# Optimization experiments

Hardware: AMD Instinct MI355X
Metric: run time of the kernel (lower is better)

The kernel has to match this reference:

```python
import jax, jax.numpy as jnp
import numpy as np

# pywt db4 decomposition low-pass filter
_DEC_LO = jnp.array([-0.010597401785069032, 0.0328830116668852, 0.030841381835560764,
                     -0.18703481171909309, -0.027983769416859854, 0.6308807679298589,
                     0.7148465705529157, 0.2303778133088965], dtype=jnp.float32)
_L = 8
_SIGN = jnp.where(jnp.arange(_L) % 2 == 0, -1.0, 1.0).astype(jnp.float32)
_DEC_HI = _SIGN * _DEC_LO[::-1]            # QMF: dec_hi[k] = (-1)^(k+1) dec_lo[L-1-k]
_REC_LO = _DEC_LO[::-1]
_REC_HI = _DEC_HI[::-1]
_LEVELS = 4


def _conv_valid(x, f):
    # x: [N, n]; true convolution (filter flipped), valid part
    k = f[::-1][None, None, :]
    return jax.lax.conv_general_dilated(x[:, None, :], k, (1,), 'VALID',
                                        dimension_numbers=('NCH', 'OIH', 'NCH'))[:, 0, :]


def _dwt(x):
    # one symmetric-mode DWT level; x: [N, n] -> (cA, cD) each [N, (n+L-1)//2]
    xp = jnp.pad(x, ((0, 0), (_L - 1, _L - 1)), mode='symmetric')
    return _conv_valid(xp, _DEC_LO)[:, 1::2], _conv_valid(xp, _DEC_HI)[:, 1::2]


def _idwt(a, d):
    # inverse DWT level; a,d: [N, m] -> [N, 2m-L+2]
    m = a.shape[-1]
    up_a = jnp.zeros((a.shape[0], 2 * m - 1), a.dtype).at[:, ::2].set(a)
    up_d = jnp.zeros((d.shape[0], 2 * m - 1), d.dtype).at[:, ::2].set(d)
    y = (_conv_valid(jnp.pad(up_a, ((0, 0), (_L - 1, _L - 1))), _REC_LO)
         + _conv_valid(jnp.pad(up_d, ((0, 0), (_L - 1, _L - 1))), _REC_HI))
    return y[:, _L - 2: y.shape[-1] - (_L - 2)]


def _wavelet_compress(x, level):
    # batched equivalent of the per-(b,c) pywt wavedec/threshold/waverec loop
    B, C, T = x.shape
    a = x.reshape(B * C, T)
    details = []
    for _ in range(_LEVELS):
        a, d = _dwt(a)
        details.append(d)
    thr = level * jnp.std(a, axis=-1, keepdims=True)  # np.std (ddof=0) of approx coeffs per row
    hard = lambda c: jnp.where(jnp.abs(c) < thr, jnp.zeros((), c.dtype), c)
    a = hard(a)
    for d in reversed(details):
        d = hard(d)
        if a.shape[-1] > d.shape[-1]:
            a = a[:, :d.shape[-1]]  # pywt waverec length alignment
        a = _idwt(a, d)
    if a.shape[-1] >= T:
        a = a[:, :T]
    else:
        a = jnp.pad(a, ((0, 0), (0, T - a.shape[-1])))
    return a.reshape(B, C, T)


def _spectral_distortion(x, key, freq_mask_prob=0.3, time_mask_prob=0.3):
    T = x.shape[-1]
    k1, k2, k3, k4 = jax.random.split(key, 4)
    X = jnp.fft.fft(x, axis=-1)
    mag, ph = jnp.abs(X), jnp.angle(X)
    idx = jnp.arange(T)
    fw = int(0.1 * T)
    f0 = jax.random.randint(k2, (), 0, T - fw)
    apply_f = jax.random.uniform(k1, ()) < freq_mask_prob
    fmask = apply_f & (idx >= f0) & (idx < f0 + fw)
    mag = mag * jnp.where(fmask, 0.1, 1.0).astype(mag.dtype)
    xd = jnp.fft.ifft(mag * jnp.exp(1j * ph), axis=-1).real.astype(x.dtype)
    tw = int(0.05 * T)
    t0 = jax.random.randint(k4, (), 0, T - tw)
    apply_t = jax.random.uniform(k3, ()) < time_mask_prob
    tmask = apply_t & (idx >= t0) & (idx < t0 + tw)
    return xd * jnp.where(tmask, 0.1, 1.0).astype(x.dtype)


def _add_noise(x, key, noise_std=0.02):
    # torch.std is unbiased -> ddof=1
    noise = jax.random.normal(key, x.shape, x.dtype) * noise_std * jnp.std(x, axis=-1, keepdims=True, ddof=1)
    return x + noise


def setup_inputs() -> dict:
    key = jax.random.key(0)
    x = jax.random.normal(key, (64, 64, 4096), dtype=jnp.float32)
    return {"x": x}


def reference(x):
    compression_level = 0.5  # fixed draw from compression_levels for determinism
    kd, kn, kcd, kcn = jax.random.split(jax.random.key(42), 4)
    compressed = _wavelet_compress(x, compression_level)
    distorted = _spectral_distortion(x, kd)
    noisy = _add_noise(x, kn)
    comb = _wavelet_compress(x, compression_level * 0.5)
    comb = _spectral_distortion(comb, kcd)
    comb = _add_noise(comb, kcn)
    # views: original, compressed, distorted, noisy, combined
    return (x, compressed, distorted, noisy, comb)
```

## Files before the change

kernel.cpp:

```cpp
#include <hip/hip_runtime.h>
#include <stdint.h>

#define T_LEN 4096
#define N_ROWS 4096
#define N_ELEM (4096u * 4096u)
#define PD(i) ((i) + ((i) >> 5))

__constant__ float c_DEC_LO[8] = {
  -0.010597401785069032f, 0.0328830116668852f, 0.030841381835560764f,
  -0.18703481171909309f, -0.027983769416859854f, 0.6308807679298589f,
   0.7148465705529157f, 0.2303778133088965f };
__constant__ float c_DEC_HI[8] = {
  -0.2303778133088965f, 0.7148465705529157f, -0.6308807679298589f,
  -0.027983769416859854f, 0.18703481171909309f, 0.030841381835560764f,
  -0.0328830116668852f, -0.010597401785069032f };

#define RL0 0.2303778133088965f
#define RL1 0.7148465705529157f
#define RL2 0.6308807679298589f
#define RL3 (-0.027983769416859854f)
#define RL4 (-0.18703481171909309f)
#define RL5 0.030841381835560764f
#define RL6 0.0328830116668852f
#define RL7 (-0.010597401785069032f)
#define RH0 (-0.010597401785069032f)
#define RH1 (-0.0328830116668852f)
#define RH2 0.030841381835560764f
#define RH3 0.18703481171909309f
#define RH4 (-0.027983769416859854f)
#define RH5 (-0.6308807679298589f)
#define RH6 0.7148465705529157f
#define RH7 (-0.2303778133088965f)

__host__ __device__ __forceinline__ uint32_t rotl32(uint32_t v, int r) {
  return (v << r) | (v >> (32 - r));
}

__host__ __device__ __forceinline__ void tf2x32(uint32_t k0, uint32_t k1,
                                                uint32_t c0, uint32_t c1,
                                                uint32_t& o0, uint32_t& o1) {
  uint32_t ks2 = k0 ^ k1 ^ 0x1BD11BDAu;
  uint32_t x0 = c0 + k0;
  uint32_t x1 = c1 + k1;
#define TFR(r) { x0 += x1; x1 = rotl32(x1, r); x1 ^= x0; }
  TFR(13) TFR(15) TFR(26) TFR(6)
  x0 += k1;  x1 += ks2 + 1u;
  TFR(17) TFR(29) TFR(16) TFR(24)
  x0 += ks2; x1 += k0 + 2u;
  TFR(13) TFR(15) TFR(26) TFR(6)
  x0 += k0;  x1 += k1 + 3u;
  TFR(17) TFR(29) TFR(16) TFR(24)
  x0 += k1;  x1 += ks2 + 4u;
  TFR(13) TFR(15) TFR(26) TFR(6)
  x0 += ks2; x1 += k0 + 5u;
#undef TFR
  o0 = x0; o1 = x1;
}

__host__ __device__ __forceinline__ uint32_t jbits_scalar(uint32_t kx, uint32_t ky) {
  uint32_t a, b; tf2x32(kx, ky, 0u, 0u, a, b);
  return a ^ b;
}

__device__ __forceinline__ uint32_t jbits_elem(uint32_t kx, uint32_t ky, uint32_t i) {
  uint32_t a, b; tf2x32(kx, ky, 0u, i, a, b); return a ^ b;
}

__host__ __device__ __forceinline__ float junif_scalar(uint32_t kx, uint32_t ky) {
  union { uint32_t u; float f; } cv;
  cv.u = (jbits_scalar(kx, ky) >> 9) | 0x3f800000u;
  return cv.f - 1.0f;
}

__host__ __device__ __forceinline__ void jsplit2(uint32_t kx, uint32_t ky, uint32_t* o) {
  tf2x32(kx, ky, 0u, 0u, o[0], o[1]);
  tf2x32(kx, ky, 0u, 1u, o[2], o[3]);
}

__host__ __device__ __forceinline__ void jsplit4(uint32_t kx, uint32_t ky, uint32_t* o) {
  tf2x32(kx, ky, 0u, 0u, o[0], o[1]);
  tf2x32(kx, ky, 0u, 1u, o[2], o[3]);
  tf2x32(kx, ky, 0u, 2u, o[4], o[5]);
  tf2x32(kx, ky, 0u, 3u, o[6], o[7]);
}

__host__ __device__ __forceinline__ int jrandint(uint32_t kx, uint32_t ky, uint32_t span) {
  uint32_t c[4];
  jsplit2(kx, ky, c);
  uint32_t hi = jbits_scalar(c[0], c[1]);
  uint32_t lo = jbits_scalar(c[2], c[3]);
  uint32_t mult = 65536u % span;
  mult = (mult * mult) % span;
  uint32_t off = ((hi % span) * mult + (lo % span)) % span;
  return (int)off;
}

__host__ __device__ void distort_params(uint32_t kx, uint32_t ky,
                                        int* f0, int* af, int* t0, int* at) {
  uint32_t q[8];
  jsplit4(kx, ky, q);
  *af = junif_scalar(q[0], q[1]) < 0.3f;
  *f0 = jrandint(q[2], q[3], 3687u);
  *at = junif_scalar(q[4], q[5]) < 0.3f;
  *t0 = jrandint(q[6], q[7], 3892u);
}

__device__ __forceinline__ float erfinv32(float x) {
  float w = -log1pf(-x * x);
  float p;
  if (w < 5.0f) {
    w = w - 2.5f;
    p = 2.81022636e-08f;
    p = fmaf(p, w, 3.43273939e-07f);
    p = fmaf(p, w, -3.5233877e-06f);
    p = fmaf(p, w, -4.39150654e-06f);
    p = fmaf(p, w, 0.00021858087f);
    p = fmaf(p, w, -0.00125372503f);
    p = fmaf(p, w, -0.00417768164f);
    p = fmaf(p, w, 0.246640727f);
    p = fmaf(p, w, 1.50140941f);
  } else {
    w = sqrtf(w) - 3.0f;
    p = -0.000200214257f;
    p = fmaf(p, w, 0.000100950558f);
    p = fmaf(p, w, 0.00134934322f);
    p = fmaf(p, w, -0.00367342844f);
    p = fmaf(p, w, 0.00573950773f);
    p = fmaf(p, w, -0.0076224613f);
    p = fmaf(p, w, 0.00943887047f);
    p = fmaf(p, w, 1.00167406f);
    p = fmaf(p, w, 2.83297682f);
  }
  return p * x;
}

__device__ __forceinline__ float jax_normal_from_bits(uint32_t bits) {
  union { uint32_t u; float f; } cv;
  cv.u = (bits >> 9) | 0x3f800000u;
  float f = cv.f - 1.0f;
  const float lo = -0.99999994f;
  float u = __fadd_rn(__fmul_rn(f, 2.0f), lo);
  u = fmaxf(lo, u);
  return 1.41421356f * erfinv32(u);
}

__device__ __forceinline__ float tree8(const float* p) {
  return __fadd_rn(
      __fadd_rn(__fadd_rn(p[0], p[1]), __fadd_rn(p[2], p[3])),
      __fadd_rn(__fadd_rn(p[4], p[5]), __fadd_rn(p[6], p[7])));
}

__device__ void dwt_step(const float* a, int n, float* oa, float* od, int nOut, int tid) {
  int iHi = (n - 2) >> 1;
  for (int i = tid; i < nOut; i += 256) {
    int base = 2 * i - 6;
    float pa[8], pd[8];
    if (i >= 3 && i <= iHi) {
      #pragma unroll
      for (int j = 0; j < 8; ++j) {
        float xv = a[base + j];
        pa[j] = __fmul_rn(c_DEC_LO[7 - j], xv);
        pd[j] = __fmul_rn(c_DEC_HI[7 - j], xv);
      }
    } else {
      #pragma unroll
      for (int j = 0; j < 8; ++j) {
        int q = base + j;
        q = (q < 0) ? (-q - 1) : ((q >= n) ? (2 * n - 1 - q) : q);
        float xv = a[q];
        pa[j] = __fmul_rn(c_DEC_LO[7 - j], xv);
        pd[j] = __fmul_rn(c_DEC_HI[7 - j], xv);
      }
    }
    oa[i] = tree8(pa);
    od[i] = tree8(pd);
  }
}

__device__ void idwt_step(const float* __restrict__ a, const float* __restrict__ d,
                          int m, float* __restrict__ out, int nOut, float thr,
                          bool trA, int tid) {
  for (int t = tid; t < nOut; t += 256) {
    int odd = t & 1;
    int h0 = (t - odd) >> 1;
    float a0 = a[h0], a1 = a[h0 + 1], a2 = a[h0 + 2], a3 = a[h0 + 3];
    if (trA) {
      a0 = (fabsf(a0) < thr) ? 0.f : a0;
      a1 = (fabsf(a1) < thr) ? 0.f : a1;
      a2 = (fabsf(a2) < thr) ? 0.f : a2;
      a3 = (fabsf(a3) < thr) ? 0.f : a3;
    }
    float d0 = d[h0], d1 = d[h0 + 1], d2 = d[h0 + 2], d3 = d[h0 + 3];
    d0 = (fabsf(d0) < thr) ? 0.f : d0;
    d1 = (fabsf(d1) < thr) ? 0.f : d1;
    d2 = (fabsf(d2) < thr) ? 0.f : d2;
    d3 = (fabsf(d3) < thr) ? 0.f : d3;
    float cl0 = odd ? RL7 : RL6, cl1 = odd ? RL5 : RL4;
    float cl2 = odd ? RL3 : RL2, cl3 = odd ? RL1 : RL0;
    float ch0 = odd ? RH7 : RH6, ch1 = odd ? RH5 : RH4;
    float ch2 = odd ? RH3 : RH2, ch3 = odd ? RH1 : RH0;
    float sa = __fadd_rn(__fadd_rn(__fmul_rn(cl0, a0), __fmul_rn(cl1, a1)),
                         __fadd_rn(__fmul_rn(cl2, a2), __fmul_rn(cl3, a3)));
    float sd = __fadd_rn(__fadd_rn(__fmul_rn(ch0, d0), __fmul_rn(ch1, d1)),
                         __fadd_rn(__fmul_rn(ch2, d2), __fmul_rn(ch3, d3)));
    out[t] = __fadd_rn(sa, sd);
  }
}

__device__ void np_pw262_partials(const float* src, float* pbuf, int tid) {
  if (tid < 24) {
    int blk = tid >> 3, k = tid & 7;
    const float* base = src + (blk == 0 ? 0 : (blk == 1 ? 128 : 192));
    int iters = (blk == 0 ? 16 : 8);
    float r = base[k];
    for (int it = 1; it < iters; ++it) r = __fadd_rn(r, base[8 * it + k]);
    pbuf[tid] = r;
  }
}

__device__ float np_pw262_combine(const float* src, const float* pbuf) {
  float b0 = tree8(pbuf + 0);
  float b1 = tree8(pbuf + 8);
  float b2 = tree8(pbuf + 16);
  for (int i = 256; i < 262; ++i) b2 = __fadd_rn(b2, src[i]);
  return __fadd_rn(b0, __fadd_rn(b1, b2));
}

__global__ __launch_bounds__(256)
void wavelet_kernel(const float* __restrict__ x, float* __restrict__ out0,
                    float* __restrict__ out1, float* __restrict__ out4,
                    int fuse, int at_c, int t0_c, uint32_t kcx, uint32_t kcy) {
  extern __shared__ float smem[];
  float* A  = smem;
  float* B  = smem + 4096;
  float* D1 = smem + 6147;
  float* D2 = smem + 8198;
  float* D3 = smem + 9227;
  float* D4 = smem + 9745;
  float* SC = smem + 10007;
  float* Bp = B + 512;
  const int row = blockIdx.x, tid = threadIdx.x;
  const float4* s4 = reinterpret_cast<const float4*>(x + (size_t)row * T_LEN);
  float4* o04 = reinterpret_cast<float4*>(out0 + (size_t)row * T_LEN);
  #pragma unroll
  for (int k = 0; k < 4; ++k) {
    float4 v = s4[tid + (k << 8)];
    *reinterpret_cast<float4*>(&A[4 * (tid + (k << 8))]) = v;
    o04[tid + (k << 8)] = v;
  }
  __syncthreads();
  dwt_step(A, 4096, B, D1, 2051, tid); __syncthreads();
  dwt_step(B, 2051, A, D2, 1029, tid); __syncthreads();
  dwt_step(A, 1029, B, D3, 518, tid);  __syncthreads();
  dwt_step(B, 518, A, D4, 262, tid);   __syncthreads();

  np_pw262_partials(A, Bp, tid);
  __syncthreads();
  if (tid == 0) SC[0] = np_pw262_combine(A, Bp) / 262.0f;
  __syncthreads();
  float mu = SC[0];
  for (int i = tid; i < 262; i += 256) {
    float dv = __fsub_rn(A[i], mu);
    B[i] = __fmul_rn(dv, dv);
  }
  __syncthreads();
  np_pw262_partials(B, Bp, tid);
  __syncthreads();
  if (tid == 0) SC[1] = __fsqrt_rn(np_pw262_combine(B, Bp) / 262.0f);
  __syncthreads();
  float sigma = SC[1];

  float ra0 = A[tid];
  float ra1 = (tid < 6) ? A[256 + tid] : 0.f;

  #pragma unroll
  for (int v = 0; v < 2; ++v) {
    if (v == 1) {
      __syncthreads();
      A[tid] = ra0;
      if (tid < 6) A[256 + tid] = ra1;
      __syncthreads();
    }
    float thr = __fmul_rn((v == 0 ? 0.5f : 0.25f), sigma);
    idwt_step(A, D4, 262, B, 518, thr, true, tid);    __syncthreads();
    idwt_step(B, D3, 518, A, 1029, thr, false, tid);  __syncthreads();
    idwt_step(A, D2, 1029, B, 2051, thr, false, tid); __syncthreads();
    idwt_step(B, D1, 2051, A, 4096, thr, false, tid); __syncthreads();
    if (v == 0) {
      float4* dst4 = reinterpret_cast<float4*>(out1 + (size_t)row * T_LEN);
      #pragma unroll
      for (int k = 0; k < 4; ++k)
        dst4[tid + (k << 8)] = *reinterpret_cast<const float4*>(&A[4 * (tid + (k << 8))]);
    }
  }

  float4* dst4 = reinterpret_cast<float4*>(out4 + (size_t)row * T_LEN);
  if (!fuse) {
    #pragma unroll
    for (int k = 0; k < 4; ++k)
      dst4[tid + (k << 8)] = *reinterpret_cast<const float4*>(&A[4 * (tid + (k << 8))]);
    return;
  }

  float w[16];
  #pragma unroll
  for (int k = 0; k < 4; ++k) {
    float4 vv = *reinterpret_cast<const float4*>(&A[4 * (tid + (k << 8))]);
    w[4 * k + 0] = vv.x; w[4 * k + 1] = vv.y; w[4 * k + 2] = vv.z; w[4 * k + 3] = vv.w;
  }
  if (at_c) {
    #pragma unroll
    for (int i = 0; i < 16; ++i) {
      int col = 4 * (tid + ((i >> 2) << 8)) + (i & 3);
      if (col >= t0_c && col < t0_c + 204) w[i] *= 0.1f;
    }
  }
  __syncthreads();
  float* red = B;
  float acc = 0.f;
  #pragma unroll
  for (int i = 0; i < 16; ++i) acc += w[i];
  red[tid] = acc; __syncthreads();
  for (int o = 128; o > 0; o >>= 1) { if (tid < o) red[tid] += red[tid + o]; __syncthreads(); }
  float nmu = red[0] * (1.0f / 4096.0f);
  __syncthreads();
  acc = 0.f;
  #pragma unroll
  for (int i = 0; i < 16; ++i) { float dv = w[i] - nmu; acc += dv * dv; }
  red[tid] = acc; __syncthreads();
  for (int o = 128; o > 0; o >>= 1) { if (tid < o) red[tid] += red[tid + o]; __syncthreads(); }
  float nsig = sqrtf(red[0] / 4095.0f);

  #pragma unroll
  for (int k = 0; k < 4; ++k) {
    float o[4];
    #pragma unroll
    for (int c = 0; c < 4; ++c) {
      uint32_t col = (uint32_t)(4 * (tid + (k << 8)) + c);
      uint32_t idx = ((uint32_t)row << 12) + col;
      float z = jax_normal_from_bits(jbits_elem(kcx, kcy, idx));
      o[c] = w[4 * k + c] + __fmul_rn(__fmul_rn(z, 0.02f), nsig);
    }
    dst4[tid + (k << 8)] = make_float4(o[0], o[1], o[2], o[3]);
  }
}

__constant__ int c_STW_OFF[6] = {0, 1024, 1280, 1344, 1360, 1364};

__global__ __launch_bounds__(256)
void distort_noise_kernel(const float* __restrict__ src, float* __restrict__ dst_d,
                          float* __restrict__ dst_n,
                          int af, int f0, int at, int t0, int nod, int wd,
                          uint32_t kx, uint32_t ky) {
  extern __shared__ float smem[];
  float* RE = smem;
  float* IM = smem + 4224;
  float2* STW = (float2*)(smem + 8448);
  const int row = blockIdx.x, tid = threadIdx.x;

  const float4* s4 = reinterpret_cast<const float4*>(src + (size_t)row * T_LEN);
  float4 v4[4];
  #pragma unroll
  for (int k = 0; k < 4; ++k) v4[k] = s4[tid + (k << 8)];

  float w[16];
  if (af) {
    for (int t = tid; t < 1365; t += 256) {
      int s, j;
      if (t < 1024) { s = 0; j = t; }
      else if (t < 1280) { s = 1; j = t - 1024; }
      else if (t < 1344) { s = 2; j = t - 1280; }
      else if (t < 1360) { s = 3; j = t - 1344; }
      else if (t < 1364) { s = 4; j = t - 1360; }
      else { s = 5; j = 0; }
      int e = j << (2 * s);
      float ang = (float)e * (-1.5339807878856412e-3f);
      float sn, cs;
      __sincosf(ang, &sn, &cs);
      STW[t] = make_float2(cs, sn);
    }
    #pragma unroll
    for (int k = 0; k < 4; ++k) {
      int p = 4 * (tid + (k << 8));
      RE[PD(p + 0)] = v4[k].x; IM[PD(p + 0)] = 0.f;
      RE[PD(p + 1)] = v4[k].y; IM[PD(p + 1)] = 0.f;
      RE[PD(p + 2)] = v4[k].z; IM[PD(p + 2)] = 0.f;
      RE[PD(p + 3)] = v4[k].w; IM[PD(p + 3)] = 0.f;
    }
    __syncthreads();
    for (int s = 0; s < 6; ++s) {
      int Lsh = 12 - 2 * s, Qsh = Lsh - 2, Qm = (1 << Qsh) - 1, off = c_STW_OFF[s];
      for (int b = tid; b < 1024; b += 256) {
        int j = b & Qm, g = b >> Qsh;
        int i0 = (g << Lsh) + j;
        int i1 = i0 + (1 << Qsh), i2 = i1 + (1 << Qsh), i3 = i2 + (1 << Qsh);
        float x0r = RE[PD(i0)], x0i = IM[PD(i0)];
        float x1r = RE[PD(i1)], x1i = IM[PD(i1)];
        float x2r = RE[PD(i2)], x2i = IM[PD(i2)];
        float x3r = RE[PD(i3)], x3i = IM[PD(i3)];
        float t0r = x0r + x2r, t0i = x0i + x2i;
        float t1r = x0r - x2r, t1i = x0i - x2i;
        float t2r = x1r + x3r, t2i = x1i + x3i;
        float t3r = x1r - x3r, t3i = x1i - x3i;
        float2 w1 = STW[off + j];
        float c1 = w1.x, s1 = w1.y;
        float c2 = c1 * c1 - s1 * s1, s2 = 2.f * c1 * s1;
        float c3 = c1 * c2 - s1 * s2, s3 = c1 * s2 + s1 * c2;
        RE[PD(i0)] = t0r + t2r; IM[PD(i0)] = t0i + t2i;
        float u1r = t1r + t3i, u1i = t1i - t3r;
        RE[PD(i1)] = u1r * c1 - u1i * s1; IM[PD(i1)] = u1r * s1 + u1i * c1;
        float u2r = t0r - t2r, u2i = t0i - t2i;
        RE[PD(i2)] = u2r * c2 - u2i * s2; IM[PD(i2)] = u2r * s2 + u2i * c2;
        float u3r = t1r - t3i, u3i = t1i + t3r;
        RE[PD(i3)] = u3r * c3 - u3i * s3; IM[PD(i3)] = u3r * s3 + u3i * c3;
      }
      __syncthreads();
    }
    for (int p = tid; p < 4096; p += 256) {
      uint32_t rb = __brev((uint32_t)p) >> 20;
      int kk = (int)(((rb & 0x555u) << 1) | ((rb >> 1) & 0x555u));
      if (kk >= f0 && kk < f0 + 409) { RE[PD(p)] *= 0.1f; IM[PD(p)] *= 0.1f; }
    }
    __syncthreads();
    for (int s = 5; s >= 0; --s) {
      int Lsh = 12 - 2 * s, Qsh = Lsh - 2, Qm = (1 << Qsh) - 1, off = c_STW_OFF[s];
      for (int b = tid; b < 1024; b += 256) {
        int j = b & Qm, g = b >> Qsh;
        int i0 = (g << Lsh) + j;
        int i1 = i0 + (1 << Qsh), i2 = i1 + (1 << Qsh), i3 = i2 + (1 << Qsh);
        float y0r = RE[PD(i0)], y0i = IM[PD(i0)];
        float y1r = RE[PD(i1)], y1i = IM[PD(i1)];
        float y2r = RE[PD(i2)], y2i = IM[PD(i2)];
        float y3r = RE[PD(i3)], y3i = IM[PD(i3)];
        float2 w1 = STW[off + j];
        float c1 = w1.x, s1 = -w1.y;
        float c2 = c1 * c1 - s1 * s1, s2 = 2.f * c1 * s1;
        float c3 = c1 * c2 - s1 * s2, s3 = c1 * s2 + s1 * c2;
        float z1r = y1r * c1 - y1i * s1, z1i = y1r * s1 + y1i * c1;
        float z2r = y2r * c2 - y2i * s2, z2i = y2r * s2 + y2i * c2;
        float z3r = y3r * c3 - y3i * s3, z3i = y3r * s3 + y3i * c3;
        float u0r = y0r + z2r, u0i = y0i + z2i;
        float u2r = y0r - z2r, u2i = y0i - z2i;
        float u1r = z1r + z3r, u1i = z1i + z3i;
        float u3r = z3i - z1i, u3i = z1r - z3r;
        RE[PD(i0)] = u0r + u1r; IM[PD(i0)] = u0i + u1i;
        RE[PD(i1)] = u2r + u3r; IM[PD(i1)] = u2i + u3i;
        RE[PD(i2)] = u0r - u1r; IM[PD(i2)] = u0i - u1i;
        RE[PD(i3)] = u2r - u3r; IM[PD(i3)] = u2i - u3i;
      }
      __syncthreads();
    }
    #pragma unroll
    for (int k = 0; k < 4; ++k) {
      int p = 4 * (tid + (k << 8));
      w[4 * k + 0] = RE[PD(p + 0)] * (1.0f / 4096.0f);
      w[4 * k + 1] = RE[PD(p + 1)] * (1.0f / 4096.0f);
      w[4 * k + 2] = RE[PD(p + 2)] * (1.0f / 4096.0f);
      w[4 * k + 3] = RE[PD(p + 3)] * (1.0f / 4096.0f);
    }
    __syncthreads();
  } else {
    #pragma unroll
    for (int k = 0; k < 4; ++k) {
      w[4 * k + 0] = v4[k].x; w[4 * k + 1] = v4[k].y;
      w[4 * k + 2] = v4[k].z; w[4 * k + 3] = v4[k].w;
    }
  }
  if (at) {
    #pragma unroll
    for (int i = 0; i < 16; ++i) {
      int col = 4 * (tid + ((i >> 2) << 8)) + (i & 3);
      if (col >= t0 && col < t0 + 204) w[i] *= 0.1f;
    }
  }
  if (wd) {
    float4* d4 = reinterpret_cast<float4*>(dst_d + (size_t)row * T_LEN);
    #pragma unroll
    for (int k = 0; k < 4; ++k)
      d4[tid + (k << 8)] = make_float4(w[4 * k], w[4 * k + 1], w[4 * k + 2], w[4 * k + 3]);
  }

  float nv[16];
  #pragma unroll
  for (int i = 0; i < 16; ++i) {
    float q;
    if (nod) q = w[i];
    else {
      float4 vv = v4[i >> 2];
      q = (i & 3) == 0 ? vv.x : (i & 3) == 1 ? vv.y : (i & 3) == 2 ? vv.z : vv.w;
    }
    nv[i] = q;
  }
  float* red = smem;
  float acc = 0.f;
  #pragma unroll
  for (int i = 0; i < 16; ++i) acc += nv[i];
  red[tid] = acc; __syncthreads();
  for (int o = 128; o > 0; o >>= 1) { if (tid < o) red[tid] += red[tid + o]; __syncthreads(); }
  float mu = red[0] * (1.0f / 4096.0f);
  __syncthreads();
  acc = 0.f;
  #pragma unroll
  for (int i = 0; i < 16; ++i) { float dv = nv[i] - mu; acc += dv * dv; }
  red[tid] = acc; __syncthreads();
  for (int o = 128; o > 0; o >>= 1) { if (tid < o) red[tid] += red[tid + o]; __syncthreads(); }
  float sigma = sqrtf(red[0] / 4095.0f);

  float4* n4 = reinterpret_cast<float4*>(dst_n + (size_t)row * T_LEN);
  #pragma unroll
  for (int k = 0; k < 4; ++k) {
    float o[4];
    #pragma unroll
    for (int c = 0; c < 4; ++c) {
      uint32_t col = (uint32_t)(4 * (tid + (k << 8)) + c);
      uint32_t idx = ((uint32_t)row << 12) + col;
      float z = jax_normal_from_bits(jbits_elem(kx, ky, idx));
      o[c] = nv[4 * k + c] + __fmul_rn(__fmul_rn(z, 0.02f), sigma);
    }
    n4[tid + (k << 8)] = make_float4(o[0], o[1], o[2], o[3]);
  }
}

extern "C" void kernel_launch(void* const* d_in, const int* in_sizes, int n_in,
                              void* d_out, int out_size, void* d_ws, size_t ws_size,
                              hipStream_t stream) {
  const float* x = (const float*)d_in[0];
  float* out = (float*)d_out;
  float* o0 = out;
  float* o1 = out + (size_t)N_ELEM;
  float* o2 = out + 2 * (size_t)N_ELEM;
  float* o3 = out + 3 * (size_t)N_ELEM;
  float* o4 = out + 4 * (size_t)N_ELEM;

  uint32_t r[8];
  jsplit4(0u, 42u, r);
  int f0d, afd, t0d, atd, f0c, afc, t0c, atc;
  distort_params(r[0], r[1], &f0d, &afd, &t0d, &atd);
  distort_params(r[4], r[5], &f0c, &afc, &t0c, &atc);

  const size_t WAVE_LDS = 10009u * 4u;
  const size_t FFT_LDS  = 11178u * 4u;

  hipLaunchKernelGGL(wavelet_kernel, dim3(N_ROWS), dim3(256), WAVE_LDS, stream,
                     x, o0, o1, o4, afc ? 0 : 1, atc, t0c, r[6], r[7]);
  hipLaunchKernelGGL(distort_noise_kernel, dim3(N_ROWS), dim3(256),
                     afd ? FFT_LDS : 1024, stream,
                     x, o2, o3, afd, f0d, atd, t0d, 0, 1, r[2], r[3]);
  if (afc) {
    hipLaunchKernelGGL(distort_noise_kernel, dim3(N_ROWS), dim3(256), FFT_LDS, stream,
                       o4, o4, o4, 1, f0c, atc, t0c, 1, 0, r[6], r[7]);
  }
}
```

Before: 333.2 us.

## Merge wavelet, distortion and noise passes into one role-split mega kernel

Replaces the separate wavelet kernel and the combined distort+noise kernel with a single 3×N_ROWS-block launch. Each block is assigned a role (wavelet, FFT distortion, or noise) interleaved by row pairs, so the noise view gets its own blocks instead of running serially after the FFT in the same block. The goal is better load balance and overlap of heterogeneous work across CUs, plus fewer launches. The cost is that every block now reserves the larger FFT LDS allocation, which can lower occupancy for the lighter roles, and x is read three times instead of twice.

```diff
diff --git a/kernel.cpp b/kernel.cpp
--- a/kernel.cpp
+++ b/kernel.cpp
@@ -226,11 +226,10 @@
   return __fadd_rn(b0, __fadd_rn(b1, b2));
 }
 
-__global__ __launch_bounds__(256)
-void wavelet_kernel(const float* __restrict__ x, float* __restrict__ out0,
-                    float* __restrict__ out1, float* __restrict__ out4,
-                    int fuse, int at_c, int t0_c, uint32_t kcx, uint32_t kcy) {
-  extern __shared__ float smem[];
+__device__ void wavelet_row(float* smem, const float* __restrict__ x,
+                            float* __restrict__ out0, float* __restrict__ out1,
+                            float* __restrict__ out4, int row,
+                            int fuse, int at_c, int t0_c, uint32_t kcx, uint32_t kcy) {
   float* A  = smem;
   float* B  = smem + 4096;
   float* D1 = smem + 6147;
@@ -239,7 +238,7 @@
   float* D4 = smem + 9745;
   float* SC = smem + 10007;
   float* Bp = B + 512;
-  const int row = blockIdx.x, tid = threadIdx.x;
+  const int tid = threadIdx.x;
   const float4* s4 = reinterpret_cast<const float4*>(x + (size_t)row * T_LEN);
   float4* o04 = reinterpret_cast<float4*>(out0 + (size_t)row * T_LEN);
   #pragma unroll
@@ -347,16 +346,13 @@
 
 __constant__ int c_STW_OFF[6] = {0, 1024, 1280, 1344, 1360, 1364};
 
-__global__ __launch_bounds__(256)
-void distort_noise_kernel(const float* __restrict__ src, float* __restrict__ dst_d,
-                          float* __restrict__ dst_n,
-                          int af, int f0, int at, int t0, int nod, int wd,
-                          uint32_t kx, uint32_t ky) {
-  extern __shared__ float smem[];
+__device__ void fft_distort_row(float* smem, const float* __restrict__ src,
+                                float* __restrict__ dst, int row,
+                                int af, int f0, int at, int t0) {
   float* RE = smem;
   float* IM = smem + 4224;
   float2* STW = (float2*)(smem + 8448);
-  const int row = blockIdx.x, tid = threadIdx.x;
+  const int tid = threadIdx.x;
 
   const float4* s4 = reinterpret_cast<const float4*>(src + (size_t)row * T_LEN);
   float4 v4[4];
@@ -458,7 +454,6 @@
       w[4 * k + 2] = RE[PD(p + 2)] * (1.0f / 4096.0f);
       w[4 * k + 3] = RE[PD(p + 3)] * (1.0f / 4096.0f);
     }
-    __syncthreads();
   } else {
     #pragma unroll
     for (int k = 0; k < 4; ++k) {
@@ -473,23 +468,25 @@
       if (col >= t0 && col < t0 + 204) w[i] *= 0.1f;
     }
   }
-  if (wd) {
-    float4* d4 = reinterpret_cast<float4*>(dst_d + (size_t)row * T_LEN);
-    #pragma unroll
-    for (int k = 0; k < 4; ++k)
-      d4[tid + (k << 8)] = make_float4(w[4 * k], w[4 * k + 1], w[4 * k + 2], w[4 * k + 3]);
-  }
-
+  float4* d4 = reinterpret_cast<float4*>(dst + (size_t)row * T_LEN);
+  #pragma unroll
+  for (int k = 0; k < 4; ++k)
+    d4[tid + (k << 8)] = make_float4(w[4 * k], w[4 * k + 1], w[4 * k + 2], w[4 * k + 3]);
+}
+
+__device__ void noise_row(float* smem, const float* __restrict__ src,
+                          float* __restrict__ dst, int row,
+                          uint32_t kx, uint32_t ky) {
+  const int tid = threadIdx.x;
+  const float4* s4 = reinterpret_cast<const float4*>(src + (size_t)row * T_LEN);
+  float4 v4[4];
+  #pragma unroll
+  for (int k = 0; k < 4; ++k) v4[k] = s4[tid + (k << 8)];
   float nv[16];
   #pragma unroll
-  for (int i = 0; i < 16; ++i) {
-    float q;
-    if (nod) q = w[i];
-    else {
-      float4 vv = v4[i >> 2];
-      q = (i & 3) == 0 ? vv.x : (i & 3) == 1 ? vv.y : (i & 3) == 2 ? vv.z : vv.w;
-    }
-    nv[i] = q;
+  for (int k = 0; k < 4; ++k) {
+    nv[4 * k + 0] = v4[k].x; nv[4 * k + 1] = v4[k].y;
+    nv[4 * k + 2] = v4[k].z; nv[4 * k + 3] = v4[k].w;
   }
   float* red = smem;
   float acc = 0.f;
@@ -506,7 +503,7 @@
   for (int o = 128; o > 0; o >>= 1) { if (tid < o) red[tid] += red[tid + o]; __syncthreads(); }
   float sigma = sqrtf(red[0] / 4095.0f);
 
-  float4* n4 = reinterpret_cast<float4*>(dst_n + (size_t)row * T_LEN);
+  float4* n4 = reinterpret_cast<float4*>(dst + (size_t)row * T_LEN);
   #pragma unroll
   for (int k = 0; k < 4; ++k) {
     float o[4];
@@ -516,6 +513,176 @@
       uint32_t idx = ((uint32_t)row << 12) + col;
       float z = jax_normal_from_bits(jbits_elem(kx, ky, idx));
       o[c] = nv[4 * k + c] + __fmul_rn(__fmul_rn(z, 0.02f), sigma);
+    }
+    n4[tid + (k << 8)] = make_float4(o[0], o[1], o[2], o[3]);
+  }
+}
+
+__global__ __launch_bounds__(256)
+void mega_kernel(const float* __restrict__ x,
+                 float* __restrict__ o0, float* __restrict__ o1,
+                 float* __restrict__ o2, float* __restrict__ o3,
+                 float* __restrict__ o4,
+                 int fuse, int at_c, int t0_c, uint32_t kcx, uint32_t kcy,
+                 int afd, int f0d, int atd, int t0d, uint32_t knx, uint32_t kny) {
+  extern __shared__ float smem[];
+  int b = blockIdx.x;
+  int role = (b >> 1) % 3;
+  int row = ((b >> 1) / 3) * 2 + (b & 1);
+  if (role == 0)
+    wavelet_row(smem, x, o0, o1, o4, row, fuse, at_c, t0_c, kcx, kcy);
+  else if (role == 1)
+    fft_distort_row(smem, x, o2, row, afd, f0d, atd, t0d);
+  else
+    noise_row(smem, x, o3, row, knx, kny);
+}
+
+__global__ __launch_bounds__(256)
+void distort_noise_kernel(const float* __restrict__ src, float* __restrict__ dst,
+                          int af, int f0, int at, int t0, uint32_t kx, uint32_t ky) {
+  extern __shared__ float smem[];
+  const int row = blockIdx.x, tid = threadIdx.x;
+  float* RE = smem;
+  float* IM = smem + 4224;
+  float2* STW = (float2*)(smem + 8448);
+  const float4* s4 = reinterpret_cast<const float4*>(src + (size_t)row * T_LEN);
+  float4 v4[4];
+  #pragma unroll
+  for (int k = 0; k < 4; ++k) v4[k] = s4[tid + (k << 8)];
+  float w[16];
+  if (af) {
+    for (int t = tid; t < 1365; t += 256) {
+      int s, j;
+      if (t < 1024) { s = 0; j = t; }
+      else if (t < 1280) { s = 1; j = t - 1024; }
+      else if (t < 1344) { s = 2; j = t - 1280; }
+      else if (t < 1360) { s = 3; j = t - 1344; }
+      else if (t < 1364) { s = 4; j = t - 1360; }
+      else { s = 5; j = 0; }
+      int e = j << (2 * s);
+      float ang = (float)e * (-1.5339807878856412e-3f);
+      float sn, cs;
+      __sincosf(ang, &sn, &cs);
+      STW[t] = make_float2(cs, sn);
+    }
+    #pragma unroll
+    for (int k = 0; k < 4; ++k) {
+      int p = 4 * (tid + (k << 8));
+      RE[PD(p + 0)] = v4[k].x; IM[PD(p + 0)] = 0.f;
+      RE[PD(p + 1)] = v4[k].y; IM[PD(p + 1)] = 0.f;
+      RE[PD(p + 2)] = v4[k].z; IM[PD(p + 2)] = 0.f;
+      RE[PD(p + 3)] = v4[k].w; IM[PD(p + 3)] = 0.f;
+    }
+    __syncthreads();
+    for (int s = 0; s < 6; ++s) {
+      int Lsh = 12 - 2 * s, Qsh = Lsh - 2, Qm = (1 << Qsh) - 1, off = c_STW_OFF[s];
+      for (int b = tid; b < 1024; b += 256) {
+        int j = b & Qm, g = b >> Qsh;
+        int i0 = (g << Lsh) + j;
+        int i1 = i0 + (1 << Qsh), i2 = i1 + (1 << Qsh), i3 = i2 + (1 << Qsh);
+        float x0r = RE[PD(i0)], x0i = IM[PD(i0)];
+        float x1r = RE[PD(i1)], x1i = IM[PD(i1)];
+        float x2r = RE[PD(i2)], x2i = IM[PD(i2)];
+        float x3r = RE[PD(i3)], x3i = IM[PD(i3)];
+        float t0r = x0r + x2r, t0i = x0i + x2i;
+        float t1r = x0r - x2r, t1i = x0i - x2i;
+        float t2r = x1r + x3r, t2i = x1i + x3i;
+        float t3r = x1r - x3r, t3i = x1i - x3i;
+        float2 w1 = STW[off + j];
+        float c1 = w1.x, s1 = w1.y;
+        float c2 = c1 * c1 - s1 * s1, s2 = 2.f * c1 * s1;
+        float c3 = c1 * c2 - s1 * s2, s3 = c1 * s2 + s1 * c2;
+        RE[PD(i0)] = t0r + t2r; IM[PD(i0)] = t0i + t2i;
+        float u1r = t1r + t3i, u1i = t1i - t3r;
+        RE[PD(i1)] = u1r * c1 - u1i * s1; IM[PD(i1)] = u1r * s1 + u1i * c1;
+        float u2r = t0r - t2r, u2i = t0i - t2i;
+        RE[PD(i2)] = u2r * c2 - u2i * s2; IM[PD(i2)] = u2r * s2 + u2i * c2;
+        float u3r = t1r - t3i, u3i = t1i + t3r;
+        RE[PD(i3)] = u3r * c3 - u3i * s3; IM[PD(i3)] = u3r * s3 + u3i * c3;
+      }
+      __syncthreads();
+    }
+    for (int p = tid; p < 4096; p += 256) {
+      uint32_t rb = __brev((uint32_t)p) >> 20;
+      int kk = (int)(((rb & 0x555u) << 1) | ((rb >> 1) & 0x555u));
+      if (kk >= f0 && kk < f0 + 409) { RE[PD(p)] *= 0.1f; IM[PD(p)] *= 0.1f; }
+    }
+    __syncthreads();
+    for (int s = 5; s >= 0; --s) {
+      int Lsh = 12 - 2 * s, Qsh = Lsh - 2, Qm = (1 << Qsh) - 1, off = c_STW_OFF[s];
+      for (int b = tid; b < 1024; b += 256) {
+        int j = b & Qm, g = b >> Qsh;
+        int i0 = (g << Lsh) + j;
+        int i1 = i0 + (1 << Qsh), i2 = i1 + (1 << Qsh), i3 = i2 + (1 << Qsh);
+        float y0r = RE[PD(i0)], y0i = IM[PD(i0)];
+        float y1r = RE[PD(i1)], y1i = IM[PD(i1)];
+        float y2r = RE[PD(i2)], y2i = IM[PD(i2)];
+        float y3r = RE[PD(i3)], y3i = IM[PD(i3)];
+        float2 w1 = STW[off + j];
+        float c1 = w1.x, s1 = -w1.y;
+        float c2 = c1 * c1 - s1 * s1, s2 = 2.f * c1 * s1;
+        float c3 = c1 * c2 - s1 * s2, s3 = c1 * s2 + s1 * c2;
+        float z1r = y1r * c1 - y1i * s1, z1i = y1r * s1 + y1i * c1;
+        float z2r = y2r * c2 - y2i * s2, z2i = y2r * s2 + y2i * c2;
+        float z3r = y3r * c3 - y3i * s3, z3i = y3r * s3 + y3i * c3;
+        float u0r = y0r + z2r, u0i = y0i + z2i;
+        float u2r = y0r - z2r, u2i = y0i - z2i;
+        float u1r = z1r + z3r, u1i = z1i + z3i;
+        float u3r = z3i - z1i, u3i = z1r - z3r;
+        RE[PD(i0)] = u0r + u1r; IM[PD(i0)] = u0i + u1i;
+        RE[PD(i1)] = u2r + u3r; IM[PD(i1)] = u2i + u3i;
+        RE[PD(i2)] = u0r - u1r; IM[PD(i2)] = u0i - u1i;
+        RE[PD(i3)] = u2r - u3r; IM[PD(i3)] = u2i - u3i;
+      }
+      __syncthreads();
+    }
+    #pragma unroll
+    for (int k = 0; k < 4; ++k) {
+      int p = 4 * (tid + (k << 8));
+      w[4 * k + 0] = RE[PD(p + 0)] * (1.0f / 4096.0f);
+      w[4 * k + 1] = RE[PD(p + 1)] * (1.0f / 4096.0f);
+      w[4 * k + 2] = RE[PD(p + 2)] * (1.0f / 4096.0f);
+      w[4 * k + 3] = RE[PD(p + 3)] * (1.0f / 4096.0f);
+    }
+    __syncthreads();
+  } else {
+    #pragma unroll
+    for (int k = 0; k < 4; ++k) {
+      w[4 * k + 0] = v4[k].x; w[4 * k + 1] = v4[k].y;
+      w[4 * k + 2] = v4[k].z; w[4 * k + 3] = v4[k].w;
+    }
+  }
+  if (at) {
+    #pragma unroll
+    for (int i = 0; i < 16; ++i) {
+      int col = 4 * (tid + ((i >> 2) << 8)) + (i & 3);
+      if (col >= t0 && col < t0 + 204) w[i] *= 0.1f;
+    }
+  }
+  float* red = smem;
+  float acc = 0.f;
+  #pragma unroll
+  for (int i = 0; i < 16; ++i) acc += w[i];
+  red[tid] = acc; __syncthreads();
+  for (int o = 128; o > 0; o >>= 1) { if (tid < o) red[tid] += red[tid + o]; __syncthreads(); }
+  float mu = red[0] * (1.0f / 4096.0f);
+  __syncthreads();
+  acc = 0.f;
+  #pragma unroll
+  for (int i = 0; i < 16; ++i) { float dv = w[i] - mu; acc += dv * dv; }
+  red[tid] = acc; __syncthreads();
+  for (int o = 128; o > 0; o >>= 1) { if (tid < o) red[tid] += red[tid + o]; __syncthreads(); }
+  float sigma = sqrtf(red[0] / 4095.0f);
+  float4* n4 = reinterpret_cast<float4*>(dst + (size_t)row * T_LEN);
+  #pragma unroll
+  for (int k = 0; k < 4; ++k) {
+    float o[4];
+    #pragma unroll
+    for (int c = 0; c < 4; ++c) {
+      uint32_t col = (uint32_t)(4 * (tid + (k << 8)) + c);
+      uint32_t idx = ((uint32_t)row << 12) + col;
+      float z = jax_normal_from_bits(jbits_elem(kx, ky, idx));
+      o[c] = w[4 * k + c] + __fmul_rn(__fmul_rn(z, 0.02f), sigma);
     }
     n4[tid + (k << 8)] = make_float4(o[0], o[1], o[2], o[3]);
   }
@@ -538,16 +705,14 @@
   distort_params(r[0], r[1], &f0d, &afd, &t0d, &atd);
   distort_params(r[4], r[5], &f0c, &afc, &t0c, &atc);
 
-  const size_t WAVE_LDS = 10009u * 4u;
-  const size_t FFT_LDS  = 11178u * 4u;
-
-  hipLaunchKernelGGL(wavelet_kernel, dim3(N_ROWS), dim3(256), WAVE_LDS, stream,
-                     x, o0, o1, o4, afc ? 0 : 1, atc, t0c, r[6], r[7]);
-  hipLaunchKernelGGL(distort_noise_kernel, dim3(N_ROWS), dim3(256),
-                     afd ? FFT_LDS : 1024, stream,
-                     x, o2, o3, afd, f0d, atd, t0d, 0, 1, r[2], r[3]);
+  const size_t MEGA_LDS = 11178u * 4u;
+
+  hipLaunchKernelGGL(mega_kernel, dim3(3 * N_ROWS), dim3(256), MEGA_LDS, stream,
+                     x, o0, o1, o2, o3, o4,
+                     afc ? 0 : 1, atc, t0c, r[6], r[7],
+                     afd, f0d, atd, t0d, r[2], r[3]);
   if (afc) {
-    hipLaunchKernelGGL(distort_noise_kernel, dim3(N_ROWS), dim3(256), FFT_LDS, stream,
-                       o4, o4, o4, 1, f0c, atc, t0c, 1, 0, r[6], r[7]);
-  }
-}
+    hipLaunchKernelGGL(distort_noise_kernel, dim3(N_ROWS), dim3(256), MEGA_LDS, stream,
+                       o4, o4, 1, f0c, atc, t0c, r[6], r[7]);
+  }
+}
```

Measured after the change: 359.4 us. +7.9%, slower.

## Compute wavelet outputs in pairs and stream final IDWT level directly

Applied to the files above, without the earlier changes.

The DWT step now has each thread compute two adjacent outputs from ten shared loads instead of sixteen and write them as float2. The IDWT step produces the even and odd output of each pair together, which removes the per-thread odd/even coefficient selects. The last IDWT level writes straight to global memory or into registers, skipping the full-row LDS round trip and one barrier. Detail buffer offsets are padded so the float2 accesses stay aligned, at the cost of float2 rather than float4 global stores in the final level.

```diff
diff --git a/kernel.cpp b/kernel.cpp
--- a/kernel.cpp
+++ b/kernel.cpp
@@ -150,60 +150,121 @@
       __fadd_rn(__fadd_rn(p[4], p[5]), __fadd_rn(p[6], p[7])));
 }
 
-__device__ void dwt_step(const float* a, int n, float* oa, float* od, int nOut, int tid) {
+__device__ __forceinline__ void dwt_one(const float* a, int n, int i,
+                                        float* oA, float* oD) {
+  int base = 2 * i - 6;
+  float pa[8], pd[8];
+  #pragma unroll
+  for (int j = 0; j < 8; ++j) {
+    int q = base + j;
+    q = (q < 0) ? (-q - 1) : ((q >= n) ? (2 * n - 1 - q) : q);
+    float xv = a[q];
+    pa[j] = __fmul_rn(c_DEC_LO[7 - j], xv);
+    pd[j] = __fmul_rn(c_DEC_HI[7 - j], xv);
+  }
+  *oA = tree8(pa); *oD = tree8(pd);
+}
+
+__device__ void dwt_step(const float* a, int n, float* oa, float* od,
+                         int nOut, int tid) {
   int iHi = (n - 2) >> 1;
-  for (int i = tid; i < nOut; i += 256) {
-    int base = 2 * i - 6;
-    float pa[8], pd[8];
-    if (i >= 3 && i <= iHi) {
+  int nPair = nOut >> 1;
+  for (int u = tid; u < nPair; u += 256) {
+    int i0 = 2 * u;
+    if (u >= 2 && (i0 + 1) <= iHi) {
+      int base = 2 * i0 - 6;
+      float x[10];
+      #pragma unroll
+      for (int j = 0; j < 10; ++j) x[j] = a[base + j];
+      float p0[8], p1[8], q0[8], q1[8];
       #pragma unroll
       for (int j = 0; j < 8; ++j) {
-        float xv = a[base + j];
-        pa[j] = __fmul_rn(c_DEC_LO[7 - j], xv);
-        pd[j] = __fmul_rn(c_DEC_HI[7 - j], xv);
+        p0[j] = __fmul_rn(c_DEC_LO[7 - j], x[j]);
+        q0[j] = __fmul_rn(c_DEC_HI[7 - j], x[j]);
+        p1[j] = __fmul_rn(c_DEC_LO[7 - j], x[j + 2]);
+        q1[j] = __fmul_rn(c_DEC_HI[7 - j], x[j + 2]);
       }
+      *reinterpret_cast<float2*>(&oa[i0]) = make_float2(tree8(p0), tree8(p1));
+      *reinterpret_cast<float2*>(&od[i0]) = make_float2(tree8(q0), tree8(q1));
     } else {
-      #pragma unroll
-      for (int j = 0; j < 8; ++j) {
-        int q = base + j;
-        q = (q < 0) ? (-q - 1) : ((q >= n) ? (2 * n - 1 - q) : q);
-        float xv = a[q];
-        pa[j] = __fmul_rn(c_DEC_LO[7 - j], xv);
-        pd[j] = __fmul_rn(c_DEC_HI[7 - j], xv);
-      }
-    }
-    oa[i] = tree8(pa);
-    od[i] = tree8(pd);
-  }
+      float a0, d0, a1, d1;
+      dwt_one(a, n, i0, &a0, &d0);
+      dwt_one(a, n, i0 + 1, &a1, &d1);
+      oa[i0] = a0; od[i0] = d0;
+      oa[i0 + 1] = a1; od[i0 + 1] = d1;
+    }
+  }
+  for (int i = 2 * nPair + tid; i < nOut; i += 256) {
+    float av, dv;
+    dwt_one(a, n, i, &av, &dv);
+    oa[i] = av; od[i] = dv;
+  }
+}
+
+__device__ __forceinline__ void idwt_pair_vals(const float* __restrict__ a,
+                                               const float* __restrict__ d,
+                                               int h, float thr, bool trA,
+                                               float* ev, float* ov) {
+  float a0 = a[h], a1 = a[h + 1], a2 = a[h + 2], a3 = a[h + 3];
+  if (trA) {
+    a0 = (fabsf(a0) < thr) ? 0.f : a0;
+    a1 = (fabsf(a1) < thr) ? 0.f : a1;
+    a2 = (fabsf(a2) < thr) ? 0.f : a2;
+    a3 = (fabsf(a3) < thr) ? 0.f : a3;
+  }
+  float d0 = d[h], d1 = d[h + 1], d2 = d[h + 2], d3 = d[h + 3];
+  d0 = (fabsf(d0) < thr) ? 0.f : d0;
+  d1 = (fabsf(d1) < thr) ? 0.f : d1;
+  d2 = (fabsf(d2) < thr) ? 0.f : d2;
+  d3 = (fabsf(d3) < thr) ? 0.f : d3;
+  float saE = __fadd_rn(__fadd_rn(__fmul_rn(RL6, a0), __fmul_rn(RL4, a1)),
+                        __fadd_rn(__fmul_rn(RL2, a2), __fmul_rn(RL0, a3)));
+  float sdE = __fadd_rn(__fadd_rn(__fmul_rn(RH6, d0), __fmul_rn(RH4, d1)),
+                        __fadd_rn(__fmul_rn(RH2, d2), __fmul_rn(RH0, d3)));
+  float saO = __fadd_rn(__fadd_rn(__fmul_rn(RL7, a0), __fmul_rn(RL5, a1)),
+                        __fadd_rn(__fmul_rn(RL3, a2), __fmul_rn(RL1, a3)));
+  float sdO = __fadd_rn(__fadd_rn(__fmul_rn(RH7, d0), __fmul_rn(RH5, d1)),
+                        __fadd_rn(__fmul_rn(RH3, d2), __fmul_rn(RH1, d3)));
+  *ev = __fadd_rn(saE, sdE);
+  *ov = __fadd_rn(saO, sdO);
 }
 
 __device__ void idwt_step(const float* __restrict__ a, const float* __restrict__ d,
-                          int m, float* __restrict__ out, int nOut, float thr,
+                          float* __restrict__ out, int nOut, float thr,
                           bool trA, int tid) {
-  for (int t = tid; t < nOut; t += 256) {
-    int odd = t & 1;
-    int h0 = (t - odd) >> 1;
-    float a0 = a[h0], a1 = a[h0 + 1], a2 = a[h0 + 2], a3 = a[h0 + 3];
-    if (trA) {
-      a0 = (fabsf(a0) < thr) ? 0.f : a0;
-      a1 = (fabsf(a1) < thr) ? 0.f : a1;
-      a2 = (fabsf(a2) < thr) ? 0.f : a2;
-      a3 = (fabsf(a3) < thr) ? 0.f : a3;
-    }
-    float d0 = d[h0], d1 = d[h0 + 1], d2 = d[h0 + 2], d3 = d[h0 + 3];
-    d0 = (fabsf(d0) < thr) ? 0.f : d0;
-    d1 = (fabsf(d1) < thr) ? 0.f : d1;
-    d2 = (fabsf(d2) < thr) ? 0.f : d2;
-    d3 = (fabsf(d3) < thr) ? 0.f : d3;
-    float cl0 = odd ? RL7 : RL6, cl1 = odd ? RL5 : RL4;
-    float cl2 = odd ? RL3 : RL2, cl3 = odd ? RL1 : RL0;
-    float ch0 = odd ? RH7 : RH6, ch1 = odd ? RH5 : RH4;
-    float ch2 = odd ? RH3 : RH2, ch3 = odd ? RH1 : RH0;
-    float sa = __fadd_rn(__fadd_rn(__fmul_rn(cl0, a0), __fmul_rn(cl1, a1)),
-                         __fadd_rn(__fmul_rn(cl2, a2), __fmul_rn(cl3, a3)));
-    float sd = __fadd_rn(__fadd_rn(__fmul_rn(ch0, d0), __fmul_rn(ch1, d1)),
-                         __fadd_rn(__fmul_rn(ch2, d2), __fmul_rn(ch3, d3)));
-    out[t] = __fadd_rn(sa, sd);
+  int nPair = nOut >> 1;
+  for (int h = tid; h < nPair; h += 256) {
+    float ev, ov;
+    idwt_pair_vals(a, d, h, thr, trA, &ev, &ov);
+    *reinterpret_cast<float2*>(&out[2 * h]) = make_float2(ev, ov);
+  }
+  if (nOut & 1) {
+    int h = nPair;
+    if (tid == (h & 255)) {
+      float ev, ov;
+      idwt_pair_vals(a, d, h, thr, trA, &ev, &ov);
+      out[2 * h] = ev;
+    }
+  }
+}
+
+__device__ void idwt_last_store(const float* __restrict__ a, const float* __restrict__ d,
+                                float thr, int tid, float* __restrict__ dstRow) {
+  #pragma unroll
+  for (int k = 0; k < 8; ++k) {
+    int h = tid + (k << 8);
+    float ev, ov;
+    idwt_pair_vals(a, d, h, thr, false, &ev, &ov);
+    *reinterpret_cast<float2*>(&dstRow[2 * h]) = make_float2(ev, ov);
+  }
+}
+
+__device__ void idwt_last_reg(const float* __restrict__ a, const float* __restrict__ d,
+                              float thr, int tid, float* w) {
+  #pragma unroll
+  for (int k = 0; k < 8; ++k) {
+    int h = tid + (k << 8);
+    idwt_pair_vals(a, d, h, thr, false, &w[2 * k], &w[2 * k + 1]);
   }
 }
 
@@ -233,11 +294,11 @@
   extern __shared__ float smem[];
   float* A  = smem;
   float* B  = smem + 4096;
-  float* D1 = smem + 6147;
-  float* D2 = smem + 8198;
-  float* D3 = smem + 9227;
-  float* D4 = smem + 9745;
-  float* SC = smem + 10007;
+  float* D1 = smem + 6148;
+  float* D2 = smem + 8200;
+  float* D3 = smem + 9230;
+  float* D4 = smem + 9748;
+  float* SC = smem + 10010;
   float* Bp = B + 512;
   const int row = blockIdx.x, tid = threadIdx.x;
   const float4* s4 = reinterpret_cast<const float4*>(x + (size_t)row * T_LEN);
@@ -273,46 +334,39 @@
   float ra0 = A[tid];
   float ra1 = (tid < 6) ? A[256 + tid] : 0.f;
 
-  #pragma unroll
-  for (int v = 0; v < 2; ++v) {
-    if (v == 1) {
-      __syncthreads();
-      A[tid] = ra0;
-      if (tid < 6) A[256 + tid] = ra1;
-      __syncthreads();
-    }
-    float thr = __fmul_rn((v == 0 ? 0.5f : 0.25f), sigma);
-    idwt_step(A, D4, 262, B, 518, thr, true, tid);    __syncthreads();
-    idwt_step(B, D3, 518, A, 1029, thr, false, tid);  __syncthreads();
-    idwt_step(A, D2, 1029, B, 2051, thr, false, tid); __syncthreads();
-    idwt_step(B, D1, 2051, A, 4096, thr, false, tid); __syncthreads();
-    if (v == 0) {
-      float4* dst4 = reinterpret_cast<float4*>(out1 + (size_t)row * T_LEN);
+  {
+    float thr = __fmul_rn(0.5f, sigma);
+    idwt_step(A, D4, B, 518, thr, true, tid);   __syncthreads();
+    idwt_step(B, D3, A, 1029, thr, false, tid); __syncthreads();
+    idwt_step(A, D2, B, 2051, thr, false, tid); __syncthreads();
+    idwt_last_store(B, D1, thr, tid, out1 + (size_t)row * T_LEN);
+    __syncthreads();
+  }
+  A[tid] = ra0;
+  if (tid < 6) A[256 + tid] = ra1;
+  __syncthreads();
+
+  float thr = __fmul_rn(0.25f, sigma);
+  idwt_step(A, D4, B, 518, thr, true, tid);   __syncthreads();
+  idwt_step(B, D3, A, 1029, thr, false, tid); __syncthreads();
+  idwt_step(A, D2, B, 2051, thr, false, tid); __syncthreads();
+
+  float* dstRow = out4 + (size_t)row * T_LEN;
+  if (!fuse) {
+    idwt_last_store(B, D1, thr, tid, dstRow);
+    return;
+  }
+
+  float w[16];
+  idwt_last_reg(B, D1, thr, tid, w);
+  if (at_c) {
+    #pragma unroll
+    for (int k = 0; k < 8; ++k) {
       #pragma unroll
-      for (int k = 0; k < 4; ++k)
-        dst4[tid + (k << 8)] = *reinterpret_cast<const float4*>(&A[4 * (tid + (k << 8))]);
-    }
-  }
-
-  float4* dst4 = reinterpret_cast<float4*>(out4 + (size_t)row * T_LEN);
-  if (!fuse) {
-    #pragma unroll
-    for (int k = 0; k < 4; ++k)
-      dst4[tid + (k << 8)] = *reinterpret_cast<const float4*>(&A[4 * (tid + (k << 8))]);
-    return;
-  }
-
-  float w[16];
-  #pragma unroll
-  for (int k = 0; k < 4; ++k) {
-    float4 vv = *reinterpret_cast<const float4*>(&A[4 * (tid + (k << 8))]);
-    w[4 * k + 0] = vv.x; w[4 * k + 1] = vv.y; w[4 * k + 2] = vv.z; w[4 * k + 3] = vv.w;
-  }
-  if (at_c) {
-    #pragma unroll
-    for (int i = 0; i < 16; ++i) {
-      int col = 4 * (tid + ((i >> 2) << 8)) + (i & 3);
-      if (col >= t0_c && col < t0_c + 204) w[i] *= 0.1f;
+      for (int c = 0; c < 2; ++c) {
+        int col = 2 * (tid + (k << 8)) + c;
+        if (col >= t0_c && col < t0_c + 204) w[2 * k + c] *= 0.1f;
+      }
     }
   }
   __syncthreads();
@@ -332,16 +386,17 @@
   float nsig = sqrtf(red[0] / 4095.0f);
 
   #pragma unroll
-  for (int k = 0; k < 4; ++k) {
-    float o[4];
-    #pragma unroll
-    for (int c = 0; c < 4; ++c) {
-      uint32_t col = (uint32_t)(4 * (tid + (k << 8)) + c);
+  for (int k = 0; k < 8; ++k) {
+    int h = tid + (k << 8);
+    float o2v[2];
+    #pragma unroll
+    for (int c = 0; c < 2; ++c) {
+      uint32_t col = (uint32_t)(2 * h + c);
       uint32_t idx = ((uint32_t)row << 12) + col;
       float z = jax_normal_from_bits(jbits_elem(kcx, kcy, idx));
-      o[c] = w[4 * k + c] + __fmul_rn(__fmul_rn(z, 0.02f), nsig);
-    }
-    dst4[tid + (k << 8)] = make_float4(o[0], o[1], o[2], o[3]);
+      o2v[c] = w[2 * k + c] + __fmul_rn(__fmul_rn(z, 0.02f), nsig);
+    }
+    *reinterpret_cast<float2*>(&dstRow[2 * h]) = make_float2(o2v[0], o2v[1]);
   }
 }
 
@@ -538,7 +593,7 @@
   distort_params(r[0], r[1], &f0d, &afd, &t0d, &atd);
   distort_params(r[4], r[5], &f0c, &afc, &t0c, &atc);
 
-  const size_t WAVE_LDS = 10009u * 4u;
+  const size_t WAVE_LDS = 10012u * 4u;
   const size_t FFT_LDS  = 11178u * 4u;
 
   hipLaunchKernelGGL(wavelet_kernel, dim3(N_ROWS), dim3(256), WAVE_LDS, stream,
```

New measurement: 329.1 us. No clear change (-1.2%).
